# Optimization experiments

Hardware: AMD Instinct MI355X
Metric: run time of the kernel (lower is better)

The kernel has to match this reference:

```python
import jax, jax.numpy as jnp
import numpy as np

N, B, K, LATENT, HIDDEN, OUT = 100000, 256, 32, 64, 256, 32


def setup_inputs() -> dict:
    key = jax.random.key(0)
    ks = jax.random.split(key, 7)
    z = jax.random.normal(ks[0], (B, K, LATENT), dtype=jnp.float32)
    s = jax.random.uniform(ks[1], (N, K), dtype=jnp.float32)
    batch = jax.random.randint(ks[2], (N,), 0, B, dtype=jnp.int64)
    W1 = jax.random.normal(ks[3], (LATENT, HIDDEN), dtype=jnp.float32) / np.sqrt(LATENT)
    b1 = jnp.zeros((HIDDEN,), dtype=jnp.float32)
    W2 = jax.random.normal(ks[4], (HIDDEN, OUT), dtype=jnp.float32) / np.sqrt(HIDDEN)
    b2 = jnp.zeros((OUT,), dtype=jnp.float32)
    return {"z": z, "s": s, "batch": batch, "W1": W1, "b1": b1, "W2": W2, "b2": b2}


def reference(z, s, batch, W1, b1, W2, b2):
    # z: [B, K, L] per-graph cluster latents; batch: [N] node->graph; s: [N, K]
    z_gather = z[batch]                                  # [N, K, L]
    node_lat = jnp.einsum("nk,nkl->nl", s, z_gather)     # [N, L]
    h = jax.nn.relu(node_lat @ W1 + b1)                  # [N, HIDDEN]
    return h @ W2 + b2                                   # [N, OUT]
```

## Files before the change

kernel.cpp:

```cpp
#include <hip/hip_runtime.h>
#include <hip/hip_fp16.h>


using f16   = _Float16;
using f16x4 = __attribute__((ext_vector_type(4))) _Float16;
using f16x8 = __attribute__((ext_vector_type(8))) _Float16;
using f32x4 = __attribute__((ext_vector_type(4))) float;

constexpr int NN     = 100000;
constexpr int KK     = 32;
constexpr int LATENT = 64;
constexpr int HIDDEN = 256;
constexpr int OUTD   = 32;

constexpr int BLOCK    = 256;
constexpr int W2F_OFF  = 16384;
constexpr int NPREP    = 25;
constexpr int SEGCAP   = 64;


__global__ __launch_bounds__(1024)
void prep(const float* __restrict__ W1,
          const float* __restrict__ W2,
          const int*   __restrict__ batch,
          f16* __restrict__ wsf,
          int* __restrict__ hist2,
          int* __restrict__ perm2) {
    __shared__ int lcnt[256];
    const int t = threadIdx.x;
    if (t < 256) lcnt[t] = 0;

    const int gid = blockIdx.x * 1024 + t;
    if (gid < 16384) {
        const int j = gid & 7, lane = (gid >> 3) & 63, g = gid >> 9;
        const int ks = g & 1, nt = g >> 1;
        const int k = ks * 32 + (lane >> 4) * 8 + j;
        const int c = nt * 16 + (lane & 15);
        wsf[gid] = (f16)W1[k * HIDDEN + c];
    } else if (gid < 16384 + 8192) {
        const int g2 = gid - 16384;
        const int j = g2 & 7, lane = (g2 >> 3) & 63, g = g2 >> 9;
        const int ks = g & 7, nt2 = g >> 3;
        const int k = ks * 32 + (lane >> 4) * 8 + j;
        const int c = nt2 * 16 + (lane & 15);
        wsf[W2F_OFF + g2] = (f16)W2[k * OUTD + c];
    }
    __syncthreads();

    const int n0 = gid * 4;
    int bb[4], slot[4];
    const bool act = n0 < NN;
    if (act) {
        const int4 bv = *(const int4*)(batch + n0);
        bb[0] = bv.x; bb[1] = bv.y; bb[2] = bv.z; bb[3] = bv.w;
        #pragma unroll
        for (int i = 0; i < 4; ++i) slot[i] = atomicAdd(&lcnt[bb[i]], 1);
    }
    if (act) {
        #pragma unroll
        for (int i = 0; i < 4; ++i)
            if (slot[i] < SEGCAP)
                perm2[(bb[i] * NPREP + blockIdx.x) * SEGCAP + slot[i]] = n0 + i;
    }
    __syncthreads();
    if (t < 256) hist2[t * 32 + blockIdx.x] = lcnt[t];
}

__global__ __launch_bounds__(BLOCK, 7)
void gnn_decoder(const float* __restrict__ z,
                 const float* __restrict__ s,
                 const f16*   __restrict__ wsf,
                 const int*   __restrict__ hist2,
                 const int*   __restrict__ perm2,
                 const float* __restrict__ b1,
                 const float* __restrict__ b2,
                 float*       __restrict__ out)
{
    __shared__ f16 zf[4][64][8];
    __shared__ f16 latlds[4][16][72];
    __shared__ f16 hcf[4][2][64][8];

    const int bg    = blockIdx.x >> 3;
    const int chunk = blockIdx.x & 7;

    const int t    = threadIdx.x;
    const int w    = t >> 6;
    const int lane = t & 63;
    const int lrow = lane & 15;
    const int quad = lane >> 4;

    const int c = (lane < NPREP) ? hist2[bg * 32 + lane] : 0;
    int x = c;
    #pragma unroll
    for (int o = 1; o < 32; o <<= 1) {
        const int y = __shfl_up(x, o);
        if (lane >= o) x += y;
    }
    const int excl  = x - c;
    const int total = __shfl(x, NPREP - 1);

    const int cnt_c = total - chunk * 64;
    if (cnt_c <= 0) return;
    const int cn = cnt_c < 64 ? cnt_c : 64;

    int gs = chunk * 64 + w * 16 + lrow;
    if (gs >= total) gs = total - 1;
    int seg = 0, base = 0;
    #pragma unroll
    for (int i = 1; i < NPREP; ++i) {
        const int si = __shfl(excl, i);
        if (gs >= si) { seg = i; base = si; }
    }
    const int pn = perm2[(bg * NPREP + seg) * SEGCAP + (gs - base)];

    f16x8 sA;
    {
        const float4* sp = (const float4*)(s + (size_t)pn * KK + quad * 8);
        const float4 s0 = sp[0], s1 = sp[1];
        sA[0] = (f16)s0.x; sA[1] = (f16)s0.y; sA[2] = (f16)s0.z; sA[3] = (f16)s0.w;
        sA[4] = (f16)s1.x; sA[5] = (f16)s1.y; sA[6] = (f16)s1.z; sA[7] = (f16)s1.w;
    }

    {
        const float* zb = z + (size_t)bg * (KK * LATENT) + quad * 8 * LATENT
                        + w * 16 + lrow;
        f16x8 v;
        #pragma unroll
        for (int j = 0; j < 8; ++j) v[j] = (f16)zb[j * LATENT];
        *(f16x8*)&zf[w][lane][0] = v;
    }
    __syncthreads();

    #pragma unroll
    for (int lt = 0; lt < 4; ++lt) {
        const f16x8 zB = *(const f16x8*)&zf[lt][lane][0];
        f32x4 D = (f32x4){0.f, 0.f, 0.f, 0.f};
        D = __builtin_amdgcn_mfma_f32_16x16x32_f16(sA, zB, D, 0, 0, 0);
        const int l = lt * 16 + lrow;
        #pragma unroll
        for (int r = 0; r < 4; ++r)
            latlds[w][quad * 4 + r][l] = (f16)D[r];
    }
    __builtin_amdgcn_wave_barrier();

    const f16x8 latB0 = *(const f16x8*)&latlds[w][lrow][quad * 8];
    const f16x8 latB1 = *(const f16x8*)&latlds[w][lrow][32 + quad * 8];

    const f16x8*  W1f = (const f16x8*)wsf;
    const f16x8*  W2f = (const f16x8*)(wsf + W2F_OFF);
    const float4* b1v = (const float4*)b1;

    f32x4 O0 = (f32x4){0.f, 0.f, 0.f, 0.f};
    f32x4 O1 = (f32x4){0.f, 0.f, 0.f, 0.f};

    #pragma unroll
    for (int ksH = 0; ksH < 8; ++ksH) {
        #pragma unroll
        for (int p = 0; p < 2; ++p) {
            const int ntA = ksH * 2 + p;
            f32x4 C = (f32x4){0.f, 0.f, 0.f, 0.f};
            C = __builtin_amdgcn_mfma_f32_16x16x32_f16(
                    W1f[(ntA * 2 + 0) * 64 + lane], latB0, C, 0, 0, 0);
            C = __builtin_amdgcn_mfma_f32_16x16x32_f16(
                    W1f[(ntA * 2 + 1) * 64 + lane], latB1, C, 0, 0, 0);
            const float4 bq = b1v[ntA * 4 + quad];
            f16x4 hv;
            hv[0] = (f16)fmaxf(C[0] + bq.x, 0.f);
            hv[1] = (f16)fmaxf(C[1] + bq.y, 0.f);
            hv[2] = (f16)fmaxf(C[2] + bq.z, 0.f);
            hv[3] = (f16)fmaxf(C[3] + bq.w, 0.f);
            *(f16x4*)&hcf[w][ksH & 1][(p * 2 + (quad >> 1)) * 16 + lrow][(quad & 1) * 4] = hv;
        }
        __builtin_amdgcn_wave_barrier();
        const f16x8 Ah = *(const f16x8*)&hcf[w][ksH & 1][lane][0];
        O0 = __builtin_amdgcn_mfma_f32_16x16x32_f16(Ah, W2f[(0 * 8 + ksH) * 64 + lane], O0, 0, 0, 0);
        O1 = __builtin_amdgcn_mfma_f32_16x16x32_f16(Ah, W2f[(1 * 8 + ksH) * 64 + lane], O1, 0, 0, 0);
    }

    {
        const float b2a = b2[lrow];
        const float b2b = b2[16 + lrow];
        #pragma unroll
        for (int r = 0; r < 4; ++r) {
            const int m = w * 16 + quad * 4 + r;
            const int pr = __shfl(pn, quad * 4 + r);
            if (m < cn) {
                float* dst = out + (size_t)pr * OUTD;
                dst[lrow]      = O0[r] + b2a;
                dst[16 + lrow] = O1[r] + b2b;
            }
        }
    }
}

extern "C" void kernel_launch(void* const* d_in, const int* in_sizes, int n_in,
                              void* d_out, int out_size, void* d_ws, size_t ws_size,
                              hipStream_t stream) {
    const float* z     = (const float*)d_in[0];
    const float* s     = (const float*)d_in[1];
    const int*   batch = (const int*)d_in[2];
    const float* W1    = (const float*)d_in[3];
    const float* b1    = (const float*)d_in[4];
    const float* W2    = (const float*)d_in[5];
    const float* b2    = (const float*)d_in[6];
    float* out = (float*)d_out;

    f16* wsf   = (f16*)d_ws;
    int* hist2 = (int*)((char*)d_ws + 49152);
    int* perm2 = hist2 + 256 * 32;

    prep<<<NPREP, 1024, 0, stream>>>(W1, W2, batch, wsf, hist2, perm2);
    gnn_decoder<<<256 * 8, BLOCK, 0, stream>>>(z, s, wsf, hist2, perm2, b1, b2, out);
}
```

Baseline: 104.1 us.

## Precompute per-graph z@W1 in prep and fold s into a single MFMA

Uses associativity to precompute z[b]@W1 (a 32x256 fp16 matrix per graph) in extra prep blocks. The main kernel then computes the hidden layer as s times zW1 in one MFMA per 16-column tile, instead of forming the latent and multiplying by W1. This removes the z load, the latent LDS staging and half the layer-1 MFMAs, but adds 4 MB of fp16 workspace traffic and one more rounding step to fp16. Block index mapping is also changed so chunks of different graphs interleave.

```diff
diff --git a/kernel.cpp b/kernel.cpp
--- a/kernel.cpp
+++ b/kernel.cpp
@@ -13,75 +13,123 @@
 constexpr int HIDDEN = 256;
 constexpr int OUTD   = 32;
 
-constexpr int BLOCK    = 256;
-constexpr int W2F_OFF  = 16384;
-constexpr int NPREP    = 25;
-constexpr int SEGCAP   = 64;
-
+constexpr int BLOCK  = 256;
+constexpr int NPREP  = 25;
+constexpr int NZBLK  = 16;
+constexpr int SEGCAP = 64;
+
+constexpr size_t ZW1_OFF  = 65536;
+constexpr size_t HIST_OFF = ZW1_OFF + (size_t)256 * 8192 * 2;
+constexpr size_t PERM_OFF = HIST_OFF + (size_t)256 * 32 * 4;
 
 __global__ __launch_bounds__(1024)
-void prep(const float* __restrict__ W1,
+void prep(const float* __restrict__ z,
+          const float* __restrict__ W1,
           const float* __restrict__ W2,
           const int*   __restrict__ batch,
-          f16* __restrict__ wsf,
+          f16* __restrict__ w2f,
+          f16* __restrict__ zw1f,
           int* __restrict__ hist2,
           int* __restrict__ perm2) {
     __shared__ int lcnt[256];
+    __shared__ f16 w1f[32 * 64 * 8];
+
     const int t = threadIdx.x;
-    if (t < 256) lcnt[t] = 0;
-
-    const int gid = blockIdx.x * 1024 + t;
-    if (gid < 16384) {
-        const int j = gid & 7, lane = (gid >> 3) & 63, g = gid >> 9;
-        const int ks = g & 1, nt = g >> 1;
-        const int k = ks * 32 + (lane >> 4) * 8 + j;
-        const int c = nt * 16 + (lane & 15);
-        wsf[gid] = (f16)W1[k * HIDDEN + c];
-    } else if (gid < 16384 + 8192) {
-        const int g2 = gid - 16384;
-        const int j = g2 & 7, lane = (g2 >> 3) & 63, g = g2 >> 9;
-        const int ks = g & 7, nt2 = g >> 3;
-        const int k = ks * 32 + (lane >> 4) * 8 + j;
-        const int c = nt2 * 16 + (lane & 15);
-        wsf[W2F_OFF + g2] = (f16)W2[k * OUTD + c];
-    }
-    __syncthreads();
-
-    const int n0 = gid * 4;
-    int bb[4], slot[4];
-    const bool act = n0 < NN;
-    if (act) {
-        const int4 bv = *(const int4*)(batch + n0);
-        bb[0] = bv.x; bb[1] = bv.y; bb[2] = bv.z; bb[3] = bv.w;
-        #pragma unroll
-        for (int i = 0; i < 4; ++i) slot[i] = atomicAdd(&lcnt[bb[i]], 1);
-    }
-    if (act) {
-        #pragma unroll
-        for (int i = 0; i < 4; ++i)
-            if (slot[i] < SEGCAP)
-                perm2[(bb[i] * NPREP + blockIdx.x) * SEGCAP + slot[i]] = n0 + i;
-    }
-    __syncthreads();
-    if (t < 256) hist2[t * 32 + blockIdx.x] = lcnt[t];
+
+    if (blockIdx.x < NPREP) {
+        if (t < 256) lcnt[t] = 0;
+        const int gid = blockIdx.x * 1024 + t;
+        if (gid < 8192) {
+            const int j = gid & 7, lane = (gid >> 3) & 63, g = gid >> 9;
+            const int ks = g & 7, o = g >> 3;
+            const int k = ks * 32 + (lane >> 4) * 8 + j;
+            const int c = o * 16 + (lane & 15);
+            w2f[gid] = (f16)W2[k * OUTD + c];
+        }
+        __syncthreads();
+
+        const int n0 = gid * 4;
+        int bb[4], slot[4];
+        const bool act = n0 < NN;
+        if (act) {
+            const int4 bv = *(const int4*)(batch + n0);
+            bb[0] = bv.x; bb[1] = bv.y; bb[2] = bv.z; bb[3] = bv.w;
+            #pragma unroll
+            for (int i = 0; i < 4; ++i) slot[i] = atomicAdd(&lcnt[bb[i]], 1);
+            #pragma unroll
+            for (int i = 0; i < 4; ++i)
+                if (slot[i] < SEGCAP)
+                    perm2[(bb[i] * NPREP + blockIdx.x) * SEGCAP + slot[i]] = n0 + i;
+        }
+        __syncthreads();
+        if (t < 256) hist2[t * 32 + blockIdx.x] = lcnt[t];
+    } else {
+        const int zb = blockIdx.x - NPREP;
+
+        #pragma unroll
+        for (int e = 0; e < 16; ++e) {
+            const int idx = e * 1024 + t;
+            const int j = idx & 7, lane = (idx >> 3) & 63, gfr = idx >> 9;
+            const int ks = gfr & 1, nt = gfr >> 1;
+            const int k = ks * 32 + (lane >> 4) * 8 + j;
+            const int c = nt * 16 + (lane & 15);
+            w1f[idx] = (f16)W1[k * HIDDEN + c];
+        }
+        __syncthreads();
+
+        const int wv   = t >> 6;
+        const int lane = t & 63;
+        const int lrow = lane & 15;
+        const int quad = lane >> 4;
+        const int g    = zb * 16 + wv;
+
+        f16x8 zA[2][2];
+        #pragma unroll
+        for (int mt = 0; mt < 2; ++mt)
+            #pragma unroll
+            for (int ks = 0; ks < 2; ++ks) {
+                const float4* zp = (const float4*)(z + (size_t)g * (KK * LATENT)
+                                   + (mt * 16 + lrow) * LATENT + ks * 32 + quad * 8);
+                const float4 a = zp[0], b = zp[1];
+                f16x8 v;
+                v[0] = (f16)a.x; v[1] = (f16)a.y; v[2] = (f16)a.z; v[3] = (f16)a.w;
+                v[4] = (f16)b.x; v[5] = (f16)b.y; v[6] = (f16)b.z; v[7] = (f16)b.w;
+                zA[mt][ks] = v;
+            }
+
+        f16* zg = zw1f + (size_t)g * 8192;
+        #pragma unroll
+        for (int nt = 0; nt < 16; ++nt) {
+            const f16x8 B0 = *(const f16x8*)&w1f[((nt * 2 + 0) * 64 + lane) * 8];
+            const f16x8 B1 = *(const f16x8*)&w1f[((nt * 2 + 1) * 64 + lane) * 8];
+            #pragma unroll
+            for (int mt = 0; mt < 2; ++mt) {
+                f32x4 D = (f32x4){0.f, 0.f, 0.f, 0.f};
+                D = __builtin_amdgcn_mfma_f32_16x16x32_f16(zA[mt][0], B0, D, 0, 0, 0);
+                D = __builtin_amdgcn_mfma_f32_16x16x32_f16(zA[mt][1], B1, D, 0, 0, 0);
+                f16x4 hv;
+                hv[0] = (f16)D[0]; hv[1] = (f16)D[1];
+                hv[2] = (f16)D[2]; hv[3] = (f16)D[3];
+                *(f16x4*)&zg[(nt * 16 + lrow) * 32 + mt * 16 + quad * 4] = hv;
+            }
+        }
+    }
 }
 
 __global__ __launch_bounds__(BLOCK, 7)
-void gnn_decoder(const float* __restrict__ z,
-                 const float* __restrict__ s,
-                 const f16*   __restrict__ wsf,
+void gnn_decoder(const float* __restrict__ s,
+                 const f16*   __restrict__ w2f,
+                 const f16*   __restrict__ zw1f,
                  const int*   __restrict__ hist2,
                  const int*   __restrict__ perm2,
                  const float* __restrict__ b1,
                  const float* __restrict__ b2,
                  float*       __restrict__ out)
 {
-    __shared__ f16 zf[4][64][8];
-    __shared__ f16 latlds[4][16][72];
     __shared__ f16 hcf[4][2][64][8];
 
-    const int bg    = blockIdx.x >> 3;
-    const int chunk = blockIdx.x & 7;
+    const int bg    = blockIdx.x & 255;
+    const int chunk = blockIdx.x >> 8;
 
     const int t    = threadIdx.x;
     const int w    = t >> 6;
@@ -121,33 +169,8 @@
         sA[4] = (f16)s1.x; sA[5] = (f16)s1.y; sA[6] = (f16)s1.z; sA[7] = (f16)s1.w;
     }
 
-    {
-        const float* zb = z + (size_t)bg * (KK * LATENT) + quad * 8 * LATENT
-                        + w * 16 + lrow;
-        f16x8 v;
-        #pragma unroll
-        for (int j = 0; j < 8; ++j) v[j] = (f16)zb[j * LATENT];
-        *(f16x8*)&zf[w][lane][0] = v;
-    }
-    __syncthreads();
-
-    #pragma unroll
-    for (int lt = 0; lt < 4; ++lt) {
-        const f16x8 zB = *(const f16x8*)&zf[lt][lane][0];
-        f32x4 D = (f32x4){0.f, 0.f, 0.f, 0.f};
-        D = __builtin_amdgcn_mfma_f32_16x16x32_f16(sA, zB, D, 0, 0, 0);
-        const int l = lt * 16 + lrow;
-        #pragma unroll
-        for (int r = 0; r < 4; ++r)
-            latlds[w][quad * 4 + r][l] = (f16)D[r];
-    }
-    __builtin_amdgcn_wave_barrier();
-
-    const f16x8 latB0 = *(const f16x8*)&latlds[w][lrow][quad * 8];
-    const f16x8 latB1 = *(const f16x8*)&latlds[w][lrow][32 + quad * 8];
-
-    const f16x8*  W1f = (const f16x8*)wsf;
-    const f16x8*  W2f = (const f16x8*)(wsf + W2F_OFF);
+    const f16* zw1g = zw1f + (size_t)bg * 8192;
+    const f16x8*  W2f = (const f16x8*)w2f;
     const float4* b1v = (const float4*)b1;
 
     f32x4 O0 = (f32x4){0.f, 0.f, 0.f, 0.f};
@@ -158,11 +181,9 @@
         #pragma unroll
         for (int p = 0; p < 2; ++p) {
             const int ntA = ksH * 2 + p;
+            const f16x8 zwA = *(const f16x8*)&zw1g[(ntA * 16 + lrow) * 32 + quad * 8];
             f32x4 C = (f32x4){0.f, 0.f, 0.f, 0.f};
-            C = __builtin_amdgcn_mfma_f32_16x16x32_f16(
-                    W1f[(ntA * 2 + 0) * 64 + lane], latB0, C, 0, 0, 0);
-            C = __builtin_amdgcn_mfma_f32_16x16x32_f16(
-                    W1f[(ntA * 2 + 1) * 64 + lane], latB1, C, 0, 0, 0);
+            C = __builtin_amdgcn_mfma_f32_16x16x32_f16(zwA, sA, C, 0, 0, 0);
             const float4 bq = b1v[ntA * 4 + quad];
             f16x4 hv;
             hv[0] = (f16)fmaxf(C[0] + bq.x, 0.f);
@@ -205,10 +226,11 @@
     const float* b2    = (const float*)d_in[6];
     float* out = (float*)d_out;
 
-    f16* wsf   = (f16*)d_ws;
-    int* hist2 = (int*)((char*)d_ws + 49152);
-    int* perm2 = hist2 + 256 * 32;
-
-    prep<<<NPREP, 1024, 0, stream>>>(W1, W2, batch, wsf, hist2, perm2);
-    gnn_decoder<<<256 * 8, BLOCK, 0, stream>>>(z, s, wsf, hist2, perm2, b1, b2, out);
+    f16* w2f   = (f16*)d_ws;
+    f16* zw1f  = (f16*)((char*)d_ws + ZW1_OFF);
+    int* hist2 = (int*)((char*)d_ws + HIST_OFF);
+    int* perm2 = (int*)((char*)d_ws + PERM_OFF);
+
+    prep<<<NPREP + NZBLK, 1024, 0, stream>>>(z, W1, W2, batch, w2f, zw1f, hist2, perm2);
+    gnn_decoder<<<256 * 8, BLOCK, 0, stream>>>(s, w2f, zw1f, hist2, perm2, b1, b2, out);
 }
```

Result: slower. 110.4 us (+6.1%).
